# Optimization experiments

Hardware: AMD Instinct MI355X
Metric: run time of the kernel (lower is better)

## Reference

```python
import jax, jax.numpy as jnp
import numpy as np
import math

B, S, D, H, DFF = 2, 2048, 1024, 16, 4096
DK = D // H
EPS = 1e-5


def setup_inputs() -> dict:
    key = jax.random.key(0)
    ks = jax.random.split(key, 8)
    s = 0.02
    return {
        "x": jax.random.normal(ks[0], (B, S, D), jnp.float32),
        "src_mask": jnp.ones((B, 1, 1, S), jnp.int32),
        "wq": jax.random.normal(ks[1], (D, D), jnp.float32) * s,
        "bq": jnp.zeros((D,), jnp.float32),
        "wk": jax.random.normal(ks[2], (D, D), jnp.float32) * s,
        "bk": jnp.zeros((D,), jnp.float32),
        "wv": jax.random.normal(ks[3], (D, D), jnp.float32) * s,
        "bv": jnp.zeros((D,), jnp.float32),
        "wo": jax.random.normal(ks[4], (D, D), jnp.float32) * s,
        "bo": jnp.zeros((D,), jnp.float32),
        "w1": jax.random.normal(ks[5], (DFF, D), jnp.float32) * s,
        "b1": jnp.zeros((DFF,), jnp.float32),
        "w2": jax.random.normal(ks[6], (D, DFF), jnp.float32) * s,
        "b2": jnp.zeros((D,), jnp.float32),
        "alpha1": jnp.ones((1,), jnp.float32),
        "bias1": jnp.ones((1,), jnp.float32),
        "alpha2": jnp.ones((1,), jnp.float32),
        "bias2": jnp.ones((1,), jnp.float32),
    }


def _layernorm(x, alpha, bias):
    # Faithful to source: unbiased std (ddof=1), divide by (std + eps),
    # scalar alpha/bias both initialized to 1.
    mean = jnp.mean(x, axis=-1, keepdims=True)
    std = jnp.std(x, axis=-1, keepdims=True, ddof=1)
    return alpha * (x - mean) / (std + EPS) + bias


def _mha(x, wq, bq, wk, bk, wv, bv, wo, bo):
    q = (x @ wq.T + bq).reshape(B, S, H, DK).swapaxes(1, 2)  # b h s d
    k = (x @ wk.T + bk).reshape(B, S, H, DK).swapaxes(1, 2)
    v = (x @ wv.T + bv).reshape(B, S, H, DK).swapaxes(1, 2)
    scores = jnp.einsum("bhqd,bhkd->bhqk", q, k) / math.sqrt(DK)
    # NOTE: source calls masked_fill (out-of-place) and discards the result,
    # so the mask has NO effect. Reproduced faithfully: no masking here.
    attn = jax.nn.softmax(scores, axis=-1)
    out = jnp.einsum("bhqk,bhkd->bhqd", attn, v)
    out = out.swapaxes(1, 2).reshape(B, S, D)
    return out @ wo.T + bo


def reference(x, src_mask, wq, bq, wk, bk, wv, bv, wo, bo,
              w1, b1, w2, b2, alpha1, bias1, alpha2, bias2):
    # residual[0]: x + attn(norm(x)) (dropout=0 -> identity)
    h1 = x + _mha(_layernorm(x, alpha1, bias1), wq, bq, wk, bk, wv, bv, wo, bo)
    # residual[1]: h1 + ffn(norm(h1))
    n2 = _layernorm(h1, alpha2, bias2)
    ffn = (n2 @ w1.T + b1) @ w2.T + b2
    return h1 + ffn
```

## Files before the change

### kernel.cpp

```cpp
#include <hip/hip_runtime.h>
#include <stdint.h>

#define Bx   2
#define Sx   2048
#define Dx   1024
#define Hx   16
#define DKx  64
#define DFFx 4096
#define Mx   4096

typedef __attribute__((ext_vector_type(8))) short short8;
typedef __attribute__((ext_vector_type(4))) float f32x4;
typedef __attribute__((ext_vector_type(4))) unsigned short ushort4v;

__device__ __forceinline__ unsigned short f2b(float f) {
    union { float f; uint32_t u; } v; v.f = f;
    uint32_t u = v.u;
    u += 0x7fffu + ((u >> 16) & 1u);
    return (unsigned short)(u >> 16);
}

__device__ __forceinline__ float fexp2(float x) {
#if __has_builtin(__builtin_amdgcn_exp2f)
    return __builtin_amdgcn_exp2f(x);
#else
    return exp2f(x);
#endif
}

__global__ __launch_bounds__(256) void conv_all(
    const float4* __restrict__ wq, const float4* __restrict__ wk,
    const float4* __restrict__ wv, const float4* __restrict__ wo,
    const float4* __restrict__ w1, const float4* __restrict__ w2,
    const float4* __restrict__ bq, const float4* __restrict__ bk,
    const float4* __restrict__ bv,
    ushort4v* __restrict__ dqkv, ushort4v* __restrict__ dwo,
    ushort4v* __restrict__ d1, ushort4v* __restrict__ d2,
    float4* __restrict__ dbias) {
    const int i = blockIdx.x * 256 + threadIdx.x;
    const int S4 = 1 << 18;
    if (i < 4 * S4) {
        const float4* s; ushort4v* d;
        if (i < S4)          { s = wq + i;            d = dqkv + i; }
        else if (i < 2 * S4) { s = wk + (i - S4);     d = dqkv + i; }
        else if (i < 3 * S4) { s = wv + (i - 2 * S4); d = dqkv + i; }
        else                 { s = wo + (i - 3 * S4); d = dwo + (i - 3 * S4); }
        const float4 v = *s;
        ushort4v o; o.x = f2b(v.x); o.y = f2b(v.y); o.z = f2b(v.z); o.w = f2b(v.w);
        *d = o;
    } else if (i < 8 * S4) {
        const float4 v = w1[i - 4 * S4];
        ushort4v o; o.x = f2b(v.x); o.y = f2b(v.y); o.z = f2b(v.z); o.w = f2b(v.w);
        d1[i - 4 * S4] = o;
    } else if (i < 12 * S4) {
        const float4 v = w2[i - 8 * S4];
        ushort4v o; o.x = f2b(v.x); o.y = f2b(v.y); o.z = f2b(v.z); o.w = f2b(v.w);
        d2[i - 8 * S4] = o;
    } else if (i < 12 * S4 + 768) {
        const int jn = i - 12 * S4;
        dbias[jn] = (jn < 256) ? bq[jn] : (jn < 512 ? bk[jn - 256] : bv[jn - 512]);
    }
}

__global__ __launch_bounds__(256) void layernorm_k(const float* __restrict__ x,
                                                   const float* __restrict__ alpha,
                                                   const float* __restrict__ beta,
                                                   unsigned short* __restrict__ out) {
    __shared__ float red[8];
    const int row = blockIdx.x;
    const int t = threadIdx.x, lane = t & 63, w = t >> 6;
    float4 v = ((const float4*)(x + (size_t)row * Dx))[t];
    float s = v.x + v.y + v.z + v.w;
    float q = v.x*v.x + v.y*v.y + v.z*v.z + v.w*v.w;
#pragma unroll
    for (int off = 1; off < 64; off <<= 1) {
        s += __shfl_xor(s, off);
        q += __shfl_xor(q, off);
    }
    if (lane == 0) { red[w] = s; red[4 + w] = q; }
    __syncthreads();
    s = red[0] + red[1] + red[2] + red[3];
    q = red[4] + red[5] + red[6] + red[7];
    const float mean = s * (1.0f / Dx);
    float var = (q - (float)Dx * mean * mean) * (1.0f / (Dx - 1));
    var = fmaxf(var, 0.0f);
    const float inv = alpha[0] / (sqrtf(var) + 1e-5f);
    const float bb = beta[0];
    ushort4v o;
    o.x = f2b((v.x - mean) * inv + bb);
    o.y = f2b((v.y - mean) * inv + bb);
    o.z = f2b((v.z - mean) * inv + bb);
    o.w = f2b((v.w - mean) * inv + bb);
    *(ushort4v*)(out + (size_t)row * Dx + t * 4) = o;
}

#define GLDS(gp, lp) __builtin_amdgcn_global_load_lds( \
    (const __attribute__((address_space(1))) unsigned int*)(gp), \
    (__attribute__((address_space(3))) unsigned int*)(lp), 16, 0, 0)

#define STAGE(buf, kt) do {                                                     \
    const int k0_ = (kt) << 5;                                                  \
    _Pragma("unroll")                                                           \
    for (int i_ = 0; i_ < MB/2 + (MB==2); ++i_) {                               \
      const int ca_ = (MB==4) ? (w*2 + i_) : w;                                 \
      GLDS(A + (size_t)(bm + ca_*16 + srow)*K + k0_ + skc*8, &As[buf][ca_*512]);\
    }                                                                           \
    _Pragma("unroll")                                                           \
    for (int i_ = 0; i_ < 2; ++i_) {                                            \
      const int cb_ = w*2 + i_;                                                 \
      GLDS(W + (size_t)(bn + cb_*16 + srow)*K + k0_ + skc*8, &Bs[buf][cb_*512]);\
    }                                                                           \
  } while (0)

template<int BM>
__global__ __launch_bounds__(256) void gemm2(const short* __restrict__ A,
                                             const short* __restrict__ W,
                                             const float* __restrict__ bias,
                                             const float* __restrict__ res,
                                             float* __restrict__ Cout,
                                             int M, int N, int K) {
    constexpr int MB = BM / 32;
    __shared__ alignas(16) short As[2][BM * 32];
    __shared__ alignas(16) short Bs[2][128 * 32];
    const int t = threadIdx.x, lane = t & 63, w = t >> 6;
    const int bb = blockIdx.x, xcd = bb & 7, jj = bb >> 3;
    const int bn = (jj & 7) * 128;
    const int bm = (xcd * 8 + (jj >> 3)) * BM;
    const int wm = (w >> 1) * (BM / 2), wn = (w & 1) * 64;
    const int srow = lane >> 2, skc = lane & 3;

    f32x4 acc[MB][4] = {};
    const int nkt = K >> 5;

    STAGE(0, 0);
    __syncthreads();
    int cur = 0;
    for (int kt = 0; kt < nkt; ++kt) {
        if (kt + 1 < nkt) STAGE(cur ^ 1, kt + 1);
        const short* as = &As[cur][0];
        const short* bs = &Bs[cur][0];
        short8 af[MB], bfr[4];
#pragma unroll
        for (int mb = 0; mb < MB; ++mb)
            af[mb] = *(const short8*)&as[(wm + mb * 16 + (lane & 15)) * 32 + (lane >> 4) * 8];
#pragma unroll
        for (int nb = 0; nb < 4; ++nb)
            bfr[nb] = *(const short8*)&bs[(wn + nb * 16 + (lane & 15)) * 32 + (lane >> 4) * 8];
#pragma unroll
        for (int mb = 0; mb < MB; ++mb)
#pragma unroll
            for (int nb = 0; nb < 4; ++nb)
                acc[mb][nb] = __builtin_amdgcn_mfma_f32_16x16x32_bf16(af[mb], bfr[nb], acc[mb][nb], 0, 0, 0);
        __syncthreads();
        cur ^= 1;
    }

    const int r0 = (lane >> 4) * 4, c0 = lane & 15;
#pragma unroll
    for (int mb = 0; mb < MB; ++mb)
#pragma unroll
        for (int nb = 0; nb < 4; ++nb) {
            const int col = bn + wn + nb * 16 + c0;
            const float bv = bias[col];
            const int row0 = bm + wm + mb * 16 + r0;
#pragma unroll
            for (int r = 0; r < 4; ++r) {
                const size_t idx = (size_t)(row0 + r) * N + col;
                Cout[idx] = acc[mb][nb][r] + bv + res[idx];
            }
        }
}

__global__ __launch_bounds__(256) void gemmsk(const short* __restrict__ A,
                                              const short* __restrict__ W,
                                              float* __restrict__ P0,
                                              float* __restrict__ P1,
                                              int K) {
    constexpr int MB = 4;
    __shared__ alignas(16) short As[2][128 * 32];
    __shared__ alignas(16) short Bs[2][128 * 32];
    const int t = threadIdx.x, lane = t & 63, w = t >> 6;
    const int bb = blockIdx.x, xcd = bb & 7, jj = bb >> 3;
    const int bn = (jj & 7) * 128;
    const int p = (xcd << 3) | (jj >> 3);
    const int bm = (p & 31) * 128;
    const int kz = p >> 5;
    float* __restrict__ P = kz ? P1 : P0;
    const int wm = (w >> 1) * 64, wn = (w & 1) * 64;
    const int srow = lane >> 2, skc = lane & 3;

    f32x4 acc[MB][4] = {};
    const int nkt = (K >> 1) >> 5;
    const int kbeg = kz * nkt;

    STAGE(0, kbeg);
    __syncthreads();
    int cur = 0;
    for (int kt = kbeg; kt < kbeg + nkt; ++kt) {
        if (kt + 1 < kbeg + nkt) STAGE(cur ^ 1, kt + 1);
        const short* as = &As[cur][0];
        const short* bs = &Bs[cur][0];
        short8 af[MB], bfr[4];
#pragma unroll
        for (int mb = 0; mb < MB; ++mb)
            af[mb] = *(const short8*)&as[(wm + mb * 16 + (lane & 15)) * 32 + (lane >> 4) * 8];
#pragma unroll
        for (int nb = 0; nb < 4; ++nb)
            bfr[nb] = *(const short8*)&bs[(wn + nb * 16 + (lane & 15)) * 32 + (lane >> 4) * 8];
#pragma unroll
        for (int mb = 0; mb < MB; ++mb)
#pragma unroll
            for (int nb = 0; nb < 4; ++nb)
                acc[mb][nb] = __builtin_amdgcn_mfma_f32_16x16x32_bf16(af[mb], bfr[nb], acc[mb][nb], 0, 0, 0);
        __syncthreads();
        cur ^= 1;
    }

    const int r0 = (lane >> 4) * 4, c0 = lane & 15;
#pragma unroll
    for (int mb = 0; mb < MB; ++mb)
#pragma unroll
        for (int nb = 0; nb < 4; ++nb) {
            const int col = bn + wn + nb * 16 + c0;
            const int row0 = bm + wm + mb * 16 + r0;
#pragma unroll
            for (int r = 0; r < 4; ++r)
                P[(size_t)(row0 + r) * Dx + col] = acc[mb][nb][r];
        }
}

__global__ __launch_bounds__(256) void epi2(const float4* __restrict__ p0,
                                            const float4* __restrict__ p1,
                                            const float4* __restrict__ b2,
                                            const float4* __restrict__ h1,
                                            float4* __restrict__ out) {
    const int i = blockIdx.x * 256 + threadIdx.x;
    const float4 bv = b2[i & 255];
    const float4 a = p0[i], b = p1[i], h = h1[i];
    float4 o;
    o.x = a.x + b.x + h.x + bv.x;
    o.y = a.y + b.y + h.y + bv.y;
    o.z = a.z + b.z + h.z + bv.z;
    o.w = a.w + b.w + h.w + bv.w;
    out[i] = o;
}

#define STG256(buf, kt) do {                                                     \
    const int k0_ = (kt) << 5;                                                   \
    _Pragma("unroll")                                                            \
    for (int i_ = 0; i_ < 2; ++i_) {                                             \
      const int c_ = i_ * 8 + w;                                                 \
      GLDS(A + (size_t)(bm + c_*16 + (lane>>2))*K + k0_ + (lane&3)*8,            \
           &As[buf][c_*512]);                                                    \
      GLDS(W + (size_t)(bn + c_*16 + (lane>>2))*K + k0_ + (lane&3)*8,            \
           &Bs[buf][c_*512]);                                                    \
    }                                                                            \
  } while (0)

template<int MODE>
__global__ __launch_bounds__(512, 2) void gemm256(const short* __restrict__ A,
                                                  const short* __restrict__ W,
                                                  const float* __restrict__ bias,
                                                  void* __restrict__ Cout,
                                                  int M, int N, int K,
                                                  int nbn, int rpx,
                                                  unsigned short* __restrict__ Qout,
                                                  unsigned short* __restrict__ Kout,
                                                  unsigned short* __restrict__ Vout) {
    __shared__ alignas(16) short As[2][256 * 32];
    __shared__ alignas(16) short Bs[2][256 * 32];
    const int t = threadIdx.x, lane = t & 63, w = t >> 6;
    const int lo = lane & 15, hi = lane >> 4;
    const int bb = blockIdx.x, xcd = bb & 7, jj = bb >> 3;
    const int bm = (xcd * rpx + jj / nbn) * 256;
    const int bn = (jj % nbn) * 256;
    const int wr = w >> 2, wc = w & 3;

    f32x4 acc[8][4] = {};
    const int nkt = K >> 5;

    STG256(0, 0);
    __syncthreads();
    int cur = 0;
    for (int kt = 0; kt < nkt; ++kt) {
        if (kt + 1 < nkt) STG256(cur ^ 1, kt + 1);
        const short* as = &As[cur][0];
        const short* bs = &Bs[cur][0];
        short8 bfr[4];
#pragma unroll
        for (int nb = 0; nb < 4; ++nb)
            bfr[nb] = *(const short8*)&bs[(wc * 64 + nb * 16 + lo) * 32 + hi * 8];
#pragma unroll
        for (int mh = 0; mh < 2; ++mh) {
            short8 af[4];
#pragma unroll
            for (int mb = 0; mb < 4; ++mb)
                af[mb] = *(const short8*)&as[(wr * 128 + mh * 64 + mb * 16 + lo) * 32 + hi * 8];
#pragma unroll
            for (int mb = 0; mb < 4; ++mb)
#pragma unroll
                for (int nb = 0; nb < 4; ++nb)
                    acc[mh * 4 + mb][nb] =
                        __builtin_amdgcn_mfma_f32_16x16x32_bf16(af[mb], bfr[nb], acc[mh * 4 + mb][nb], 0, 0, 0);
        }
        __syncthreads();
        cur ^= 1;
    }

#pragma unroll
    for (int mb = 0; mb < 8; ++mb)
#pragma unroll
        for (int nb = 0; nb < 4; ++nb) {
            const int col = bn + wc * 64 + nb * 16 + lo;
            const float bv = bias[col];
            const int row0 = bm + wr * 128 + mb * 16 + hi * 4;
            if (MODE == 0) {
#pragma unroll
                for (int r = 0; r < 4; ++r)
                    ((unsigned short*)Cout)[(size_t)(row0 + r) * N + col] = f2b(acc[mb][nb][r] + bv);
            } else {
                if (col < 1024) {
#pragma unroll
                    for (int r = 0; r < 4; ++r)
                        Qout[(size_t)(row0 + r) * 1024 + col] = f2b(acc[mb][nb][r] + bv);
                } else if (col < 2048) {
#pragma unroll
                    for (int r = 0; r < 4; ++r)
                        Kout[(size_t)(row0 + r) * 1024 + (col - 1024)] = f2b(acc[mb][nb][r] + bv);
                } else {
                    const int dk = col - 2048, hh = dk >> 6, dlo = dk & 63;
                    const int bbv = row0 >> 11, s0 = row0 & 2047;
                    const int vrow = (bbv * 16 + hh) * 64 + dlo;
                    ushort4v pv;
                    pv.x = f2b(acc[mb][nb][0] + bv);
                    pv.y = f2b(acc[mb][nb][1] + bv);
                    pv.z = f2b(acc[mb][nb][2] + bv);
                    pv.w = f2b(acc[mb][nb][3] + bv);
                    *(ushort4v*)&Vout[(size_t)vrow * Sx + s0] = pv;
                }
            }
        }
}

__global__ __launch_bounds__(256) void attn_fwd3(const short* __restrict__ Q,
                                                 const short* __restrict__ Kg,
                                                 const short* __restrict__ Vtg,
                                                 unsigned short* __restrict__ O) {
    __shared__ alignas(16) short Ks[64 * 64];
    __shared__ alignas(16) short Vs[64 * 64];
    __shared__ alignas(16) short Pl[4][16 * 64];
    const int t = threadIdx.x, lane = t & 63, w = t >> 6;
    const int bh = blockIdx.x;
    const int b = bh >> 4, h = bh & 15;
    const int q0 = blockIdx.y * 64 + w * 16;
    const int lo = lane & 15, hi = lane >> 4;

    short8 qf[2];
#pragma unroll
    for (int kf = 0; kf < 2; ++kf)
        qf[kf] = *(const short8*)&Q[(size_t)(b * Sx + q0 + lo) * Dx + h * DKx + kf * 32 + hi * 8];

    f32x4 o_[4] = {};
    f32x4 l_acc = {};
    short8 ones;
#pragma unroll
    for (int j = 0; j < 8; ++j) ones[j] = (short)0x3F80;

    const int srow = t >> 2;
    const int scol2 = (t & 3) * 32;
    const int swz = (srow & 7) << 4;
    const short* Kbase = Kg + (size_t)(b * Sx) * Dx + h * DKx;
    const short* Vbase = Vtg + (size_t)(bh * 64 + srow) * Sx;
    char* KsB = (char*)Ks;
    char* VsB = (char*)Vs;
    char* PwB = (char*)&Pl[w][0];

    short8 kr0, kr1, vr0, vr1;
    {
        const short* kp = Kbase + (size_t)srow * Dx + (t & 3) * 16;
        kr0 = *(const short8*)kp; kr1 = *(const short8*)(kp + 8);
        const short* vp = Vbase + (t & 3) * 16;
        vr0 = *(const short8*)vp; vr1 = *(const short8*)(vp + 8);
    }

    const float cexp = 0.18033688011112042f;

    for (int kt = 0; kt < Sx / 64; ++kt) {
        __syncthreads();
        *(short8*)(KsB + ((srow * 128 + scol2) ^ swz)) = kr0;
        *(short8*)(KsB + ((srow * 128 + scol2 + 16) ^ swz)) = kr1;
        *(short8*)(VsB + ((srow * 128 + scol2) ^ swz)) = vr0;
        *(short8*)(VsB + ((srow * 128 + scol2 + 16) ^ swz)) = vr1;
        __syncthreads();
        if (kt + 1 < Sx / 64) {
            const short* kp = Kbase + (size_t)((kt + 1) * 64 + srow) * Dx + (t & 3) * 16;
            kr0 = *(const short8*)kp; kr1 = *(const short8*)(kp + 8);
            const short* vp = Vbase + (kt + 1) * 64 + (t & 3) * 16;
            vr0 = *(const short8*)vp; vr1 = *(const short8*)(vp + 8);
        }

        f32x4 s[4] = {};
#pragma unroll
        for (int nb = 0; nb < 4; ++nb) {
            const int key = nb * 16 + lo;
            const int ksw = (key & 7) << 4;
#pragma unroll
            for (int kf = 0; kf < 2; ++kf) {
                const short8 kfr = *(const short8*)(KsB + ((key * 128 + kf * 64 + hi * 16) ^ ksw));
                s[nb] = __builtin_amdgcn_mfma_f32_16x16x32_bf16(qf[kf], kfr, s[nb], 0, 0, 0);
            }
        }

#pragma unroll
        for (int nb = 0; nb < 4; ++nb) {
            const int k = nb * 16 + lo;
#pragma unroll
            for (int r = 0; r < 4; ++r) {
                const float p = fexp2(s[nb][r] * cexp);
                union { float f; uint32_t u; } cv; cv.f = p;
                const int qq = hi * 4 + r;
                *(short*)(PwB + ((qq * 128 + k * 2) ^ ((qq & 7) << 4))) = (short)(cv.u >> 16);
            }
        }

        short8 pa[2];
#pragma unroll
        for (int kc = 0; kc < 2; ++kc)
            pa[kc] = *(const short8*)(PwB + ((lo * 128 + kc * 64 + hi * 16) ^ ((lo & 7) << 4)));

        l_acc = __builtin_amdgcn_mfma_f32_16x16x32_bf16(pa[0], ones, l_acc, 0, 0, 0);
        l_acc = __builtin_amdgcn_mfma_f32_16x16x32_bf16(pa[1], ones, l_acc, 0, 0, 0);

#pragma unroll
        for (int d = 0; d < 4; ++d) {
            const int vd = d * 16 + lo;
            const int vsw = (vd & 7) << 4;
#pragma unroll
            for (int kc = 0; kc < 2; ++kc) {
                const short8 vf = *(const short8*)(VsB + ((vd * 128 + kc * 64 + hi * 16) ^ vsw));
                o_[d] = __builtin_amdgcn_mfma_f32_16x16x32_bf16(pa[kc], vf, o_[d], 0, 0, 0);
            }
        }
    }

#pragma unroll
    for (int d = 0; d < 4; ++d)
#pragma unroll
        for (int r = 0; r < 4; ++r) {
            const int qrow = b * Sx + q0 + hi * 4 + r;
            O[(size_t)qrow * Dx + h * DKx + d * 16 + lo] = f2b(o_[d][r] / l_acc[r]);
        }
}

extern "C" void kernel_launch(void* const* d_in, const int* in_sizes, int n_in,
                              void* d_out, int out_size, void* d_ws, size_t ws_size,
                              hipStream_t stream) {
    const float* x  = (const float*)d_in[0];
    const float* wq = (const float*)d_in[2];
    const float* bq = (const float*)d_in[3];
    const float* wk = (const float*)d_in[4];
    const float* bk = (const float*)d_in[5];
    const float* wv = (const float*)d_in[6];
    const float* bv = (const float*)d_in[7];
    const float* wo = (const float*)d_in[8];
    const float* bo = (const float*)d_in[9];
    const float* w1 = (const float*)d_in[10];
    const float* b1 = (const float*)d_in[11];
    const float* w2 = (const float*)d_in[12];
    const float* b2 = (const float*)d_in[13];
    const float* alpha1 = (const float*)d_in[14];
    const float* bias1  = (const float*)d_in[15];
    const float* alpha2 = (const float*)d_in[16];
    const float* bias2  = (const float*)d_in[17];
    float* out = (float*)d_out;

    short* ws   = (short*)d_ws;
    short* wqkv = ws;
    short* wob  = wqkv + 3145728;
    short* w1b  = wob  + 1048576;
    short* w2b  = w1b  + 4194304;
    short* n1   = w2b  + 4194304;
    short* Qb   = n1   + 4194304;
    short* Kb   = Qb   + 4194304;
    short* Vt   = Kb   + 4194304;
    short* f1   = Vt   + 4194304;
    float* h1   = (float*)(f1 + 16777216);
    float* bqkv = (float*)((char*)h1 + ((size_t)Mx * Dx * 4));
    short* ao = n1;
    short* n2 = n1;
    float* p0 = (float*)n1;
    float* p1 = (float*)Kb;

    conv_all<<<12291, 256, 0, stream>>>((const float4*)wq, (const float4*)wk,
                                        (const float4*)wv, (const float4*)wo,
                                        (const float4*)w1, (const float4*)w2,
                                        (const float4*)bq, (const float4*)bk,
                                        (const float4*)bv,
                                        (ushort4v*)wqkv, (ushort4v*)wob,
                                        (ushort4v*)w1b, (ushort4v*)w2b,
                                        (float4*)bqkv);

    layernorm_k<<<Mx, 256, 0, stream>>>(x, alpha1, bias1, (unsigned short*)n1);

    gemm256<2><<<192, 512, 0, stream>>>(n1, wqkv, bqkv, nullptr,
                                        Mx, 3072, Dx, 12, 2,
                                        (unsigned short*)Qb, (unsigned short*)Kb,
                                        (unsigned short*)Vt);

    attn_fwd3<<<dim3(32, 32), 256, 0, stream>>>(Qb, Kb, Vt, (unsigned short*)ao);

    gemm2<64><<<512, 256, 0, stream>>>(ao, wob, bo, x, h1, Mx, Dx, Dx);

    layernorm_k<<<Mx, 256, 0, stream>>>(h1, alpha2, bias2, (unsigned short*)n2);

    gemm256<0><<<256, 512, 0, stream>>>(n2, w1b, b1, f1,
                                        Mx, DFFx, Dx, 16, 2, nullptr, nullptr, nullptr);

    gemmsk<<<512, 256, 0, stream>>>(f1, w2b, p0, p1, DFFx);
    epi2<<<4096, 256, 0, stream>>>((const float4*)p0, (const float4*)p1,
                                   (const float4*)b2, (const float4*)h1, (float4*)out);
}
```

Measured before the change: 377.5 us.

## Replace 256-tile GEMMs with 128-tile kernel and widen attention query tile

Swaps the 256x256 GEMM kernel for a 128x128 tiled kernel with XCD-aware block mapping, used for both the QKV and FFN1 projections, which raises the block count. The softmax scale is folded into Q in the QKV epilogue, so the exp loop no longer multiplies by it. The attention kernel now gives each wave 32 query rows instead of 16, reusing each K/V fragment across two MFMA row blocks, and wraps the MFMA phases in s_setprio. It also fixes the STAGE loop count for MB==2. The smaller GEMM tiles trade less data reuse per block for better occupancy and load balance, and the wider attention tile costs more registers per wave.

```diff
diff --git a/kernel.cpp b/kernel.cpp
--- a/kernel.cpp
+++ b/kernel.cpp
@@ -8,6 +8,8 @@
 #define DKx  64
 #define DFFx 4096
 #define Mx   4096
+
+#define CEXP 0.18033688011112042f
 
 typedef __attribute__((ext_vector_type(8))) short short8;
 typedef __attribute__((ext_vector_type(4))) float f32x4;
@@ -101,7 +103,7 @@
 #define STAGE(buf, kt) do {                                                     \
     const int k0_ = (kt) << 5;                                                  \
     _Pragma("unroll")                                                           \
-    for (int i_ = 0; i_ < MB/2 + (MB==2); ++i_) {                               \
+    for (int i_ = 0; i_ < MB/2; ++i_) {                                         \
       const int ca_ = (MB==4) ? (w*2 + i_) : w;                                 \
       GLDS(A + (size_t)(bm + ca_*16 + srow)*K + k0_ + skc*8, &As[buf][ca_*512]);\
     }                                                                           \
@@ -167,6 +169,88 @@
             for (int r = 0; r < 4; ++r) {
                 const size_t idx = (size_t)(row0 + r) * N + col;
                 Cout[idx] = acc[mb][nb][r] + bv + res[idx];
+            }
+        }
+}
+
+template<int MODE>
+__global__ __launch_bounds__(256) void gemm128(const short* __restrict__ A,
+                                               const short* __restrict__ W,
+                                               const float* __restrict__ bias,
+                                               void* __restrict__ Cout,
+                                               int N, int K,
+                                               unsigned short* __restrict__ Qout,
+                                               unsigned short* __restrict__ Kout,
+                                               unsigned short* __restrict__ Vout) {
+    constexpr int MB = 4;
+    __shared__ alignas(16) short As[2][128 * 32];
+    __shared__ alignas(16) short Bs[2][128 * 32];
+    const int t = threadIdx.x, lane = t & 63, w = t >> 6;
+    const int bb = blockIdx.x, bpx = gridDim.x >> 3;
+    const int g = (bb & 7) * bpx + (bb >> 3);
+    const int bn = (g >> 5) * 128;
+    const int bm = (g & 31) * 128;
+    const int wm = (w >> 1) * 64, wn = (w & 1) * 64;
+    const int srow = lane >> 2, skc = lane & 3;
+
+    f32x4 acc[MB][4] = {};
+    const int nkt = K >> 5;
+
+    STAGE(0, 0);
+    __syncthreads();
+    int cur = 0;
+    for (int kt = 0; kt < nkt; ++kt) {
+        if (kt + 1 < nkt) STAGE(cur ^ 1, kt + 1);
+        const short* as = &As[cur][0];
+        const short* bs = &Bs[cur][0];
+        short8 af[MB], bfr[4];
+#pragma unroll
+        for (int mb = 0; mb < MB; ++mb)
+            af[mb] = *(const short8*)&as[(wm + mb * 16 + (lane & 15)) * 32 + (lane >> 4) * 8];
+#pragma unroll
+        for (int nb = 0; nb < 4; ++nb)
+            bfr[nb] = *(const short8*)&bs[(wn + nb * 16 + (lane & 15)) * 32 + (lane >> 4) * 8];
+#pragma unroll
+        for (int mb = 0; mb < MB; ++mb)
+#pragma unroll
+            for (int nb = 0; nb < 4; ++nb)
+                acc[mb][nb] = __builtin_amdgcn_mfma_f32_16x16x32_bf16(af[mb], bfr[nb], acc[mb][nb], 0, 0, 0);
+        __syncthreads();
+        cur ^= 1;
+    }
+
+    const int r0 = (lane >> 4) * 4, c0 = lane & 15;
+#pragma unroll
+    for (int mb = 0; mb < MB; ++mb)
+#pragma unroll
+        for (int nb = 0; nb < 4; ++nb) {
+            const int col = bn + wn + nb * 16 + c0;
+            const float bv = bias[col];
+            const int row0 = bm + wm + mb * 16 + r0;
+            if (MODE == 0) {
+#pragma unroll
+                for (int r = 0; r < 4; ++r)
+                    ((unsigned short*)Cout)[(size_t)(row0 + r) * N + col] = f2b(acc[mb][nb][r] + bv);
+            } else {
+                if (col < 1024) {
+#pragma unroll
+                    for (int r = 0; r < 4; ++r)
+                        Qout[(size_t)(row0 + r) * 1024 + col] = f2b((acc[mb][nb][r] + bv) * CEXP);
+                } else if (col < 2048) {
+#pragma unroll
+                    for (int r = 0; r < 4; ++r)
+                        Kout[(size_t)(row0 + r) * 1024 + (col - 1024)] = f2b(acc[mb][nb][r] + bv);
+                } else {
+                    const int dk = col - 2048, hh = dk >> 6, dlo = dk & 63;
+                    const int bbv = row0 >> 11, s0 = row0 & 2047;
+                    const int vrow = (bbv * 16 + hh) * 64 + dlo;
+                    ushort4v pv;
+                    pv.x = f2b(acc[mb][nb][0] + bv);
+                    pv.y = f2b(acc[mb][nb][1] + bv);
+                    pv.z = f2b(acc[mb][nb][2] + bv);
+                    pv.w = f2b(acc[mb][nb][3] + bv);
+                    *(ushort4v*)&Vout[(size_t)vrow * Sx + s0] = pv;
+                }
             }
         }
 }
@@ -245,123 +329,29 @@
     out[i] = o;
 }
 
-#define STG256(buf, kt) do {                                                     \
-    const int k0_ = (kt) << 5;                                                   \
-    _Pragma("unroll")                                                            \
-    for (int i_ = 0; i_ < 2; ++i_) {                                             \
-      const int c_ = i_ * 8 + w;                                                 \
-      GLDS(A + (size_t)(bm + c_*16 + (lane>>2))*K + k0_ + (lane&3)*8,            \
-           &As[buf][c_*512]);                                                    \
-      GLDS(W + (size_t)(bn + c_*16 + (lane>>2))*K + k0_ + (lane&3)*8,            \
-           &Bs[buf][c_*512]);                                                    \
-    }                                                                            \
-  } while (0)
-
-template<int MODE>
-__global__ __launch_bounds__(512, 2) void gemm256(const short* __restrict__ A,
-                                                  const short* __restrict__ W,
-                                                  const float* __restrict__ bias,
-                                                  void* __restrict__ Cout,
-                                                  int M, int N, int K,
-                                                  int nbn, int rpx,
-                                                  unsigned short* __restrict__ Qout,
-                                                  unsigned short* __restrict__ Kout,
-                                                  unsigned short* __restrict__ Vout) {
-    __shared__ alignas(16) short As[2][256 * 32];
-    __shared__ alignas(16) short Bs[2][256 * 32];
-    const int t = threadIdx.x, lane = t & 63, w = t >> 6;
-    const int lo = lane & 15, hi = lane >> 4;
-    const int bb = blockIdx.x, xcd = bb & 7, jj = bb >> 3;
-    const int bm = (xcd * rpx + jj / nbn) * 256;
-    const int bn = (jj % nbn) * 256;
-    const int wr = w >> 2, wc = w & 3;
-
-    f32x4 acc[8][4] = {};
-    const int nkt = K >> 5;
-
-    STG256(0, 0);
-    __syncthreads();
-    int cur = 0;
-    for (int kt = 0; kt < nkt; ++kt) {
-        if (kt + 1 < nkt) STG256(cur ^ 1, kt + 1);
-        const short* as = &As[cur][0];
-        const short* bs = &Bs[cur][0];
-        short8 bfr[4];
-#pragma unroll
-        for (int nb = 0; nb < 4; ++nb)
-            bfr[nb] = *(const short8*)&bs[(wc * 64 + nb * 16 + lo) * 32 + hi * 8];
-#pragma unroll
-        for (int mh = 0; mh < 2; ++mh) {
-            short8 af[4];
-#pragma unroll
-            for (int mb = 0; mb < 4; ++mb)
-                af[mb] = *(const short8*)&as[(wr * 128 + mh * 64 + mb * 16 + lo) * 32 + hi * 8];
-#pragma unroll
-            for (int mb = 0; mb < 4; ++mb)
-#pragma unroll
-                for (int nb = 0; nb < 4; ++nb)
-                    acc[mh * 4 + mb][nb] =
-                        __builtin_amdgcn_mfma_f32_16x16x32_bf16(af[mb], bfr[nb], acc[mh * 4 + mb][nb], 0, 0, 0);
-        }
-        __syncthreads();
-        cur ^= 1;
-    }
-
-#pragma unroll
-    for (int mb = 0; mb < 8; ++mb)
-#pragma unroll
-        for (int nb = 0; nb < 4; ++nb) {
-            const int col = bn + wc * 64 + nb * 16 + lo;
-            const float bv = bias[col];
-            const int row0 = bm + wr * 128 + mb * 16 + hi * 4;
-            if (MODE == 0) {
-#pragma unroll
-                for (int r = 0; r < 4; ++r)
-                    ((unsigned short*)Cout)[(size_t)(row0 + r) * N + col] = f2b(acc[mb][nb][r] + bv);
-            } else {
-                if (col < 1024) {
-#pragma unroll
-                    for (int r = 0; r < 4; ++r)
-                        Qout[(size_t)(row0 + r) * 1024 + col] = f2b(acc[mb][nb][r] + bv);
-                } else if (col < 2048) {
-#pragma unroll
-                    for (int r = 0; r < 4; ++r)
-                        Kout[(size_t)(row0 + r) * 1024 + (col - 1024)] = f2b(acc[mb][nb][r] + bv);
-                } else {
-                    const int dk = col - 2048, hh = dk >> 6, dlo = dk & 63;
-                    const int bbv = row0 >> 11, s0 = row0 & 2047;
-                    const int vrow = (bbv * 16 + hh) * 64 + dlo;
-                    ushort4v pv;
-                    pv.x = f2b(acc[mb][nb][0] + bv);
-                    pv.y = f2b(acc[mb][nb][1] + bv);
-                    pv.z = f2b(acc[mb][nb][2] + bv);
-                    pv.w = f2b(acc[mb][nb][3] + bv);
-                    *(ushort4v*)&Vout[(size_t)vrow * Sx + s0] = pv;
-                }
-            }
-        }
-}
-
-__global__ __launch_bounds__(256) void attn_fwd3(const short* __restrict__ Q,
+__global__ __launch_bounds__(256) void attn_fwd4(const short* __restrict__ Q,
                                                  const short* __restrict__ Kg,
                                                  const short* __restrict__ Vtg,
                                                  unsigned short* __restrict__ O) {
     __shared__ alignas(16) short Ks[64 * 64];
     __shared__ alignas(16) short Vs[64 * 64];
-    __shared__ alignas(16) short Pl[4][16 * 64];
+    __shared__ alignas(16) short Pl[4][32 * 64];
     const int t = threadIdx.x, lane = t & 63, w = t >> 6;
     const int bh = blockIdx.x;
     const int b = bh >> 4, h = bh & 15;
-    const int q0 = blockIdx.y * 64 + w * 16;
+    const int q0 = blockIdx.y * 128 + w * 32;
     const int lo = lane & 15, hi = lane >> 4;
 
-    short8 qf[2];
-#pragma unroll
-    for (int kf = 0; kf < 2; ++kf)
-        qf[kf] = *(const short8*)&Q[(size_t)(b * Sx + q0 + lo) * Dx + h * DKx + kf * 32 + hi * 8];
-
-    f32x4 o_[4] = {};
-    f32x4 l_acc = {};
+    short8 qf[2][2];
+#pragma unroll
+    for (int mb = 0; mb < 2; ++mb)
+#pragma unroll
+        for (int kf = 0; kf < 2; ++kf)
+            qf[mb][kf] = *(const short8*)&Q[(size_t)(b * Sx + q0 + mb * 16 + lo) * Dx
+                                            + h * DKx + kf * 32 + hi * 8];
+
+    f32x4 o_[2][4] = {};
+    f32x4 l_acc[2] = {};
     short8 ones;
 #pragma unroll
     for (int j = 0; j < 8; ++j) ones[j] = (short)0x3F80;
@@ -382,8 +372,6 @@
         const short* vp = Vbase + (t & 3) * 16;
         vr0 = *(const short8*)vp; vr1 = *(const short8*)(vp + 8);
     }
-
-    const float cexp = 0.18033688011112042f;
 
     for (int kt = 0; kt < Sx / 64; ++kt) {
         __syncthreads();
@@ -399,7 +387,8 @@
             vr0 = *(const short8*)vp; vr1 = *(const short8*)(vp + 8);
         }
 
-        f32x4 s[4] = {};
+        f32x4 s[2][4] = {};
+        __builtin_amdgcn_s_setprio(1);
 #pragma unroll
         for (int nb = 0; nb < 4; ++nb) {
             const int key = nb * 16 + lo;
@@ -407,29 +396,40 @@
 #pragma unroll
             for (int kf = 0; kf < 2; ++kf) {
                 const short8 kfr = *(const short8*)(KsB + ((key * 128 + kf * 64 + hi * 16) ^ ksw));
-                s[nb] = __builtin_amdgcn_mfma_f32_16x16x32_bf16(qf[kf], kfr, s[nb], 0, 0, 0);
+#pragma unroll
+                for (int mb = 0; mb < 2; ++mb)
+                    s[mb][nb] = __builtin_amdgcn_mfma_f32_16x16x32_bf16(qf[mb][kf], kfr, s[mb][nb], 0, 0, 0);
             }
         }
-
-#pragma unroll
-        for (int nb = 0; nb < 4; ++nb) {
-            const int k = nb * 16 + lo;
-#pragma unroll
-            for (int r = 0; r < 4; ++r) {
-                const float p = fexp2(s[nb][r] * cexp);
-                union { float f; uint32_t u; } cv; cv.f = p;
-                const int qq = hi * 4 + r;
-                *(short*)(PwB + ((qq * 128 + k * 2) ^ ((qq & 7) << 4))) = (short)(cv.u >> 16);
+        __builtin_amdgcn_s_setprio(0);
+
+#pragma unroll
+        for (int mb = 0; mb < 2; ++mb)
+#pragma unroll
+            for (int nb = 0; nb < 4; ++nb) {
+                const int k = nb * 16 + lo;
+#pragma unroll
+                for (int r = 0; r < 4; ++r) {
+                    const float p = fexp2(s[mb][nb][r]);
+                    union { float f; uint32_t u; } cv; cv.f = p;
+                    const int qq = mb * 16 + hi * 4 + r;
+                    *(short*)(PwB + ((qq * 128 + k * 2) ^ ((qq & 7) << 4))) = (short)(cv.u >> 16);
+                }
             }
-        }
-
-        short8 pa[2];
-#pragma unroll
-        for (int kc = 0; kc < 2; ++kc)
-            pa[kc] = *(const short8*)(PwB + ((lo * 128 + kc * 64 + hi * 16) ^ ((lo & 7) << 4)));
-
-        l_acc = __builtin_amdgcn_mfma_f32_16x16x32_bf16(pa[0], ones, l_acc, 0, 0, 0);
-        l_acc = __builtin_amdgcn_mfma_f32_16x16x32_bf16(pa[1], ones, l_acc, 0, 0, 0);
+
+        short8 pa[2][2];
+#pragma unroll
+        for (int mb = 0; mb < 2; ++mb)
+#pragma unroll
+            for (int kc = 0; kc < 2; ++kc)
+                pa[mb][kc] = *(const short8*)(PwB + (((mb * 16 + lo) * 128 + kc * 64 + hi * 16) ^ ((lo & 7) << 4)));
+
+        __builtin_amdgcn_s_setprio(1);
+#pragma unroll
+        for (int mb = 0; mb < 2; ++mb) {
+            l_acc[mb] = __builtin_amdgcn_mfma_f32_16x16x32_bf16(pa[mb][0], ones, l_acc[mb], 0, 0, 0);
+            l_acc[mb] = __builtin_amdgcn_mfma_f32_16x16x32_bf16(pa[mb][1], ones, l_acc[mb], 0, 0, 0);
+        }
 
 #pragma unroll
         for (int d = 0; d < 4; ++d) {
@@ -438,18 +438,23 @@
 #pragma unroll
             for (int kc = 0; kc < 2; ++kc) {
                 const short8 vf = *(const short8*)(VsB + ((vd * 128 + kc * 64 + hi * 16) ^ vsw));
-                o_[d] = __builtin_amdgcn_mfma_f32_16x16x32_bf16(pa[kc], vf, o_[d], 0, 0, 0);
+#pragma unroll
+                for (int mb = 0; mb < 2; ++mb)
+                    o_[mb][d] = __builtin_amdgcn_mfma_f32_16x16x32_bf16(pa[mb][kc], vf, o_[mb][d], 0, 0, 0);
             }
         }
-    }
-
-#pragma unroll
-    for (int d = 0; d < 4; ++d)
-#pragma unroll
-        for (int r = 0; r < 4; ++r) {
-            const int qrow = b * Sx + q0 + hi * 4 + r;
-            O[(size_t)qrow * Dx + h * DKx + d * 16 + lo] = f2b(o_[d][r] / l_acc[r]);
-        }
+        __builtin_amdgcn_s_setprio(0);
+    }
+
+#pragma unroll
+    for (int mb = 0; mb < 2; ++mb)
+#pragma unroll
+        for (int d = 0; d < 4; ++d)
+#pragma unroll
+            for (int r = 0; r < 4; ++r) {
+                const int qrow = b * Sx + q0 + mb * 16 + hi * 4 + r;
+                O[(size_t)qrow * Dx + h * DKx + d * 16 + lo] = f2b(o_[mb][d][r] / l_acc[mb][r]);
+            }
 }
 
 extern "C" void kernel_launch(void* const* d_in, const int* in_sizes, int n_in,
@@ -502,19 +507,18 @@
 
     layernorm_k<<<Mx, 256, 0, stream>>>(x, alpha1, bias1, (unsigned short*)n1);
 
-    gemm256<2><<<192, 512, 0, stream>>>(n1, wqkv, bqkv, nullptr,
-                                        Mx, 3072, Dx, 12, 2,
+    gemm128<2><<<768, 256, 0, stream>>>(n1, wqkv, bqkv, nullptr, 3072, Dx,
                                         (unsigned short*)Qb, (unsigned short*)Kb,
                                         (unsigned short*)Vt);
 
-    attn_fwd3<<<dim3(32, 32), 256, 0, stream>>>(Qb, Kb, Vt, (unsigned short*)ao);
+    attn_fwd4<<<dim3(32, 16), 256, 0, stream>>>(Qb, Kb, Vt, (unsigned short*)ao);
 
     gemm2<64><<<512, 256, 0, stream>>>(ao, wob, bo, x, h1, Mx, Dx, Dx);
 
     layernorm_k<<<Mx, 256, 0, stream>>>(h1, alpha2, bias2, (unsigned short*)n2);
 
-    gemm256<0><<<256, 512, 0, stream>>>(n2, w1b, b1, f1,
-                                        Mx, DFFx, Dx, 16, 2, nullptr, nullptr, nullptr);
+    gemm128<0><<<1024, 256, 0, stream>>>(n2, w1b, b1, f1, DFFx, Dx,
+                                         nullptr, nullptr, nullptr);
 
     gemmsk<<<512, 256, 0, stream>>>(f1, w2b, p0, p1, DFFx);
     epi2<<<4096, 256, 0, stream>>>((const float4*)p0, (const float4*)p1,
```

Result: faster. 366.6 us (-2.9%).
